# Performance work log

Hardware: AMD Instinct MI355X
Metric: run time of the kernel (lower is better)

Reference implementation:

```python
import jax, jax.numpy as jnp
import numpy as np

B, S, D, H = 4, 2048, 1024, 16
DH = D // H  # 64


def setup_inputs() -> dict:
    key = jax.random.key(0)
    ks = jax.random.split(key, 9)
    scale = 1.0 / np.sqrt(D)
    x = jax.random.normal(ks[0], (B, S, D), dtype=jnp.float32)
    # Stacked per-head projection weights, equivalent to ModuleList of Linear(D, DH)
    Wq = jax.random.uniform(ks[1], (H, D, DH), jnp.float32, -scale, scale)
    bq = jax.random.uniform(ks[2], (H, DH), jnp.float32, -scale, scale)
    Wk = jax.random.uniform(ks[3], (H, D, DH), jnp.float32, -scale, scale)
    bk = jax.random.uniform(ks[4], (H, DH), jnp.float32, -scale, scale)
    Wv = jax.random.uniform(ks[5], (H, D, DH), jnp.float32, -scale, scale)
    bv = jax.random.uniform(ks[6], (H, DH), jnp.float32, -scale, scale)
    Wo = jax.random.uniform(ks[7], (D, D), jnp.float32, -scale, scale)
    bo = jax.random.uniform(ks[8], (D,), jnp.float32, -scale, scale)
    return {"x": x, "Wq": Wq, "bq": bq, "Wk": Wk, "bk": bk,
            "Wv": Wv, "bv": bv, "Wo": Wo, "bo": bo}


def reference(x, Wq, bq, Wk, bk, Wv, bv, Wo, bo):
    # Per-head Linear projections, batched across heads: [B,S,D]x[H,D,DH] -> [B,H,S,DH]
    q = jnp.einsum('bsd,hde->bhse', x, Wq) + bq[None, :, None, :]
    k = jnp.einsum('bsd,hde->bhse', x, Wk) + bk[None, :, None, :]
    v = jnp.einsum('bsd,hde->bhse', x, Wv) + bv[None, :, None, :]
    # Scaled dot-product attention (no mask is applied in the original forward)
    scores = jnp.einsum('bhse,bhte->bhst', q, k) / jnp.sqrt(jnp.float32(DH))
    attn = jax.nn.softmax(scores, axis=-1)
    z = jnp.einsum('bhst,bhte->bhse', attn, v)  # [B,H,S,DH]
    # Concat heads on last dim (head-major order matches torch.cat over dim=-1)
    multihead = jnp.transpose(z, (0, 2, 1, 3)).reshape(B, S, D)
    return multihead @ Wo + bo
```

## Files before the change

kernel.cpp:

```cpp
#include <hip/hip_runtime.h>
#include <hip/hip_bf16.h>
#include <cstdint>
#include <cstddef>


typedef unsigned short u16;
typedef unsigned int u32;
typedef __attribute__((ext_vector_type(8))) __bf16 bf16x8;
typedef __attribute__((ext_vector_type(8))) unsigned short u16x8;
typedef __attribute__((ext_vector_type(4))) float f32x4;
typedef __attribute__((ext_vector_type(4))) unsigned int u32x4;

__device__ __forceinline__ u16 f2bf(float f) {
  union { __hip_bfloat16 h; u16 u; } c;
  c.h = __float2bfloat16(f);
  return c.u;
}
__device__ __forceinline__ u32 pk2c(float a, float b) {
  const u32 ua = __float_as_uint(a);
  const u32 ub = __float_as_uint(b);
  const u32 ra = ua + 0x7FFFu + ((ua >> 16) & 1u);
  const u32 rb = ub + 0x7FFFu + ((ub >> 16) & 1u);
  return (ra >> 16) | (rb & 0xFFFF0000u);
}
__device__ __forceinline__ float ex2(float x) {
  return __builtin_amdgcn_exp2f(x);
}

__device__ __forceinline__ void async16(const void* g, void* l) {
  __builtin_amdgcn_global_load_lds(
      (const __attribute__((address_space(1))) void*)g,
      (__attribute__((address_space(3))) void*)l, 16, 0, 0);
}

__global__ void k_pack_all(const float* __restrict__ x,
                           const float* __restrict__ Wq, const float* __restrict__ Wk,
                           const float* __restrict__ Wv,
                           const float* __restrict__ bq, const float* __restrict__ bk,
                           const float* __restrict__ bv,
                           const float* __restrict__ Wo,
                           u16* __restrict__ xb, u16* __restrict__ Wt,
                           float* __restrict__ bqkv, u16* __restrict__ Wot) {
  const int bid = blockIdx.x;
  if (bid < 8192) {
    const int i = (bid * 256 + threadIdx.x) * 4;
    const float4 v = *(const float4*)(x + i);
    ushort4 o;
    o.x = f2bf(v.x); o.y = f2bf(v.y); o.z = f2bf(v.z); o.w = f2bf(v.w);
    *(ushort4*)(xb + i) = o;
  } else if (bid < 11264) {
    const int gid = (bid - 8192) * 256 + threadIdx.x;
    const int n = gid >> 8;
    const int d0 = (gid & 255) << 2;
    const int proj = n >> 10, rem = n & 1023, h = rem >> 6, e = rem & 63;
    const float* Wp = (proj == 0) ? Wq : ((proj == 1) ? Wk : Wv);
    const float* src = Wp + h * 65536 + e;
    ushort4 o;
    o.x = f2bf(src[(d0 + 0) * 64]);
    o.y = f2bf(src[(d0 + 1) * 64]);
    o.z = f2bf(src[(d0 + 2) * 64]);
    o.w = f2bf(src[(d0 + 3) * 64]);
    *(ushort4*)(Wt + (size_t)n * 1024 + d0) = o;
  } else if (bid < 11276) {
    const int n = (bid - 11264) * 256 + threadIdx.x;
    const int proj = n >> 10, rem = n & 1023, h = rem >> 6, e = rem & 63;
    const float* bp = (proj == 0) ? bq : ((proj == 1) ? bk : bv);
    bqkv[n] = bp[h * 64 + e];
  } else {
    const int gid = (bid - 11276) * 256 + threadIdx.x;
    const int n = gid >> 8;
    const int d0 = (gid & 255) << 2;
    ushort4 o;
    o.x = f2bf(Wo[(size_t)(d0 + 0) * 1024 + n]);
    o.y = f2bf(Wo[(size_t)(d0 + 1) * 1024 + n]);
    o.z = f2bf(Wo[(size_t)(d0 + 2) * 1024 + n]);
    o.w = f2bf(Wo[(size_t)(d0 + 3) * 1024 + n]);
    *(ushort4*)(Wot + (size_t)n * 1024 + d0) = o;
  }
}

template <int MODE>
__global__ __launch_bounds__(256)
void k_gemm(const u16* __restrict__ A, const u16* __restrict__ Bt,
            const float* __restrict__ bias, void* __restrict__ Cout, int ldc) {
  __shared__ __align__(16) u16 Alds[128 * 32];
  __shared__ __align__(16) u16 Blds[128 * 32];
  const int t = threadIdx.x;
  const int lane = t & 63;
  const int w = t >> 6;
  const int l15 = lane & 15;
  const int quad = lane >> 4;
  const int wm = w >> 1, wn = w & 1;
  const int m0 = blockIdx.y << 7;
  const int n0 = blockIdx.x << 7;

  const u16* ga0 = A + (size_t)(m0 + (t >> 2)) * 1024 + (t & 3) * 8;
  const u16* ga1 = ga0 + (size_t)64 * 1024;
  const u16* gb0 = Bt + (size_t)(n0 + (t >> 2)) * 1024 + (t & 3) * 8;
  const u16* gb1 = gb0 + (size_t)64 * 1024;
  u16* const lA0 = Alds + w * 512;
  u16* const lA1 = Alds + w * 512 + 2048;
  u16* const lB0 = Blds + w * 512;
  u16* const lB1 = Blds + w * 512 + 2048;

  f32x4 acc[4][4];
#pragma unroll
  for (int mi = 0; mi < 4; ++mi)
#pragma unroll
    for (int ni = 0; ni < 4; ++ni) acc[mi][ni] = (f32x4){0.f, 0.f, 0.f, 0.f};

  for (int k0 = 0; k0 < 1024; k0 += 32) {
    __syncthreads();
    async16(ga0, lA0); async16(ga1, lA1);
    async16(gb0, lB0); async16(gb1, lB1);
    ga0 += 32; ga1 += 32; gb0 += 32; gb1 += 32;
    __syncthreads();
    bf16x8 af[4], bfr[4];
#pragma unroll
    for (int i = 0; i < 4; ++i) {
      af[i]  = *(const bf16x8*)(Alds + (wm * 64 + i * 16 + l15) * 32 + quad * 8);
      bfr[i] = *(const bf16x8*)(Blds + (wn * 64 + i * 16 + l15) * 32 + quad * 8);
    }
#pragma unroll
    for (int mi = 0; mi < 4; ++mi)
#pragma unroll
      for (int ni = 0; ni < 4; ++ni)
        acc[mi][ni] = __builtin_amdgcn_mfma_f32_16x16x32_bf16(af[mi], bfr[ni], acc[mi][ni], 0, 0, 0);
  }

  const int row0 = m0 + wm * 64;
  const int col0 = n0 + wn * 64;
  const float qscale = (MODE == 0 && col0 < 1024) ? 0.125f * 1.4426950408889634f : 1.0f;
#pragma unroll
  for (int mi = 0; mi < 4; ++mi) {
#pragma unroll
    for (int ni = 0; ni < 4; ++ni) {
      const int col = col0 + ni * 16 + l15;
      const float bb = bias[col];
#pragma unroll
      for (int r = 0; r < 4; ++r) {
        const int row = row0 + mi * 16 + quad * 4 + r;
        const float v = (acc[mi][ni][r] + bb) * qscale;
        if (MODE == 0) ((u16*)Cout)[(size_t)row * ldc + col] = f2bf(v);
        else           ((float*)Cout)[(size_t)row * ldc + col] = v;
      }
    }
  }
}

__global__ __launch_bounds__(256)
void k_vt(const u16* __restrict__ qkv, u16* __restrict__ vtg) {
  __shared__ u16 tile[64][72];
  const int t = threadIdx.x;
  const int bh = blockIdx.y, b = bh >> 4, h = bh & 15;
  const int s0 = blockIdx.x << 6;
  {
    const int row = t >> 2, col0 = (t & 3) * 16;
    const u16* src = qkv + (size_t)(b * 2048 + s0 + row) * 3072 + 2048 + h * 64 + col0;
    const u16x8 v0 = *(const u16x8*)src;
    const u16x8 v1 = *(const u16x8*)(src + 8);
    *(u16x8*)&tile[row][col0] = v0;
    *(u16x8*)&tile[row][col0 + 8] = v1;
  }
  __syncthreads();
  {
    const int e = t >> 2, sc = (t & 3) * 16;
    u16 buf[16];
#pragma unroll
    for (int i = 0; i < 16; ++i) buf[i] = tile[sc + i][e];
    u16* dst = vtg + ((size_t)bh * 64 + e) * 2048 + s0 + sc;
    *(u16x8*)dst = *(const u16x8*)&buf[0];
    *(u16x8*)(dst + 8) = *(const u16x8*)&buf[8];
  }
}

__global__ __launch_bounds__(256)
void k_attn(const u16* __restrict__ qkv, const u16* __restrict__ vtg,
            u16* __restrict__ mh) {
  __shared__ __align__(16) u16 smem[16384];
  u16* const Klds = smem;
  u16* const Vlds = smem + 8192;

  const int t = threadIdx.x;
  const int lane = t & 63;
  const int w = t >> 6;
  const int l15 = lane & 15;
  const int quad = lane >> 4;
  const int bh = blockIdx.y, b = bh >> 4, h = bh & 15;
  const int s0 = blockIdx.x << 7;

  const int lam0 = t >> 3;
  const int key0 = (lam0 & 3) | (((lam0 >> 2) & 3) << 3) | (((lam0 >> 4) & 1) << 2);
  const int ck = (t & 7) ^ (lam0 & 7);
  const u16* kbase = qkv + (size_t)(b * 2048 + key0) * 3072 + 1024 + h * 64 + ck * 8;
  const int e0 = t >> 4;
  const int cv = (t & 15) ^ e0;
  const u16* vbase = vtg + ((size_t)bh * 64 + e0) * 2048 + cv * 8;
  u16* const KldsW = Klds + w * 512;
  u16* const VldsW = Vlds + w * 512;

  bf16x8 aq[2][2];
#pragma unroll
  for (int g = 0; g < 2; ++g)
#pragma unroll
    for (int ks2 = 0; ks2 < 2; ++ks2)
      aq[g][ks2] = *(const bf16x8*)(qkv +
          (size_t)(b * 2048 + s0 + w * 32 + g * 16 + l15) * 3072 +
          h * 64 + ks2 * 32 + quad * 8);

  const u32x4 onesu = (u32x4){0x3F803F80u, 0x3F803F80u, 0x3F803F80u, 0x3F803F80u};
  const bf16x8 ones = __builtin_bit_cast(bf16x8, onesu);

  f32x4 o[2][4];
  f32x4 lacc[2];
#pragma unroll
  for (int g = 0; g < 2; ++g) {
    lacc[g] = (f32x4){0.f, 0.f, 0.f, 0.f};
#pragma unroll
    for (int ne = 0; ne < 4; ++ne) o[g][ne] = (f32x4){0.f, 0.f, 0.f, 0.f};
  }

  for (int kt = 0; kt < 16; ++kt) {
    __syncthreads();
#pragma unroll
    for (int r = 0; r < 4; ++r)
      async16(kbase + r * (32 * 3072), KldsW + r * 2048);
#pragma unroll
    for (int r = 0; r < 4; ++r)
      async16(vbase + r * (16 * 2048), VldsW + r * 2048);
    kbase += 128 * 3072;
    vbase += 128;
    __syncthreads();

#pragma unroll
    for (int ks = 0; ks < 4; ++ks) {
      u32x4 pf[2];
#pragma unroll
      for (int h2 = 0; h2 < 2; ++h2) {
        const int kt8 = ks * 2 + h2;
        const int row = kt8 * 16 + l15;
        const bf16x8 kf0 = *(const bf16x8*)(Klds + row * 64 + ((quad) ^ (l15 & 7)) * 8);
        const bf16x8 kf1 = *(const bf16x8*)(Klds + row * 64 + ((4 + quad) ^ (l15 & 7)) * 8);
        f32x4 st[2];
#pragma unroll
        for (int g = 0; g < 2; ++g) {
          st[g] = __builtin_amdgcn_mfma_f32_16x16x32_bf16(kf0, aq[g][0], (f32x4){0.f,0.f,0.f,0.f}, 0, 0, 0);
          st[g] = __builtin_amdgcn_mfma_f32_16x16x32_bf16(kf1, aq[g][1], st[g], 0, 0, 0);
        }
#pragma unroll
        for (int g = 0; g < 2; ++g) {
          const float p0 = ex2(st[g][0]), p1 = ex2(st[g][1]);
          const float p2 = ex2(st[g][2]), p3 = ex2(st[g][3]);
          pf[g][h2 * 2 + 0] = pk2c(p0, p1);
          pf[g][h2 * 2 + 1] = pk2c(p2, p3);
        }
      }
#pragma unroll
      for (int ne = 0; ne < 4; ++ne) {
        const int e = ne * 16 + l15;
        const bf16x8 bv8 = *(const bf16x8*)(Vlds + e * 128 + (((ks * 4 + quad) ^ l15) & 15) * 8);
#pragma unroll
        for (int g = 0; g < 2; ++g)
          o[g][ne] = __builtin_amdgcn_mfma_f32_16x16x32_bf16(
              __builtin_bit_cast(bf16x8, pf[g]), bv8, o[g][ne], 0, 0, 0);
      }
#pragma unroll
      for (int g = 0; g < 2; ++g)
        lacc[g] = __builtin_amdgcn_mfma_f32_16x16x32_bf16(
            __builtin_bit_cast(bf16x8, pf[g]), ones, lacc[g], 0, 0, 0);
    }
  }

#pragma unroll
  for (int g = 0; g < 2; ++g) {
#pragma unroll
    for (int r = 0; r < 4; ++r) {
      const float iv = 1.f / lacc[g][r];
      const int row = s0 + w * 32 + g * 16 + quad * 4 + r;
#pragma unroll
      for (int ne = 0; ne < 4; ++ne) {
        const int col = h * 64 + ne * 16 + l15;
        mh[(size_t)(b * 2048 + row) * 1024 + col] = f2bf(o[g][ne][r] * iv);
      }
    }
  }
}

extern "C" void kernel_launch(void* const* d_in, const int* in_sizes, int n_in,
                              void* d_out, int out_size, void* d_ws, size_t ws_size,
                              hipStream_t stream) {
  (void)in_sizes; (void)n_in; (void)out_size; (void)ws_size;
  const float* x  = (const float*)d_in[0];
  const float* Wq = (const float*)d_in[1];
  const float* bq = (const float*)d_in[2];
  const float* Wk = (const float*)d_in[3];
  const float* bk = (const float*)d_in[4];
  const float* Wv = (const float*)d_in[5];
  const float* bv = (const float*)d_in[6];
  const float* Wo = (const float*)d_in[7];
  const float* bo = (const float*)d_in[8];

  char* ws = (char*)d_ws;
  u16*   Xb   = (u16*)  (ws + 0);
  u16*   Vtg  = (u16*)  (ws + 0);
  u16*   Wt   = (u16*)  (ws + 16777216);
  float* bqkv = (float*)(ws + 23068672);
  u16*   Wot  = (u16*)  (ws + 23080960);
  u16*   QKV  = (u16*)  (ws + 25178112);
  u16*   MH   = (u16*)  (ws + 75509760);
  float* out  = (float*)d_out;

  k_pack_all <<<12300, 256, 0, stream>>>(x, Wq, Wk, Wv, bq, bk, bv, Wo,
                                         Xb, Wt, bqkv, Wot);
  k_gemm<0>  <<<dim3(24, 64), 256, 0, stream>>>(Xb, Wt, bqkv, (void*)QKV, 3072);
  k_vt       <<<dim3(32, 64), 256, 0, stream>>>(QKV, Vtg);
  k_attn     <<<dim3(16, 64), 256, 0, stream>>>(QKV, Vtg, MH);
  k_gemm<1>  <<<dim3(8, 64), 256, 0, stream>>>(MH, Wot, bo, (void*)out, 1024);
}
```

Before: 319.5 us.

## Transpose weights via LDS tiles, use packed bf16 convert, reorder attention grid

The weight pack step now transposes Wq/Wk/Wv and Wo through a 64x64 shared-memory tile, so global reads and writes are coalesced instead of strided scalar loads. The bf16 pair-pack helper uses the hardware packed-convert builtin when the compiler provides it. The attention grid is swapped so that consecutive blocks cover different (batch, head) pairs for the same query tile, which changes how work is spread across CUs and what the caches see. Rounding behavior of the builtin may differ slightly from the manual rounding on special values.

After: 291.7 us. 8.7% less time.

```diff
diff --git a/kernel.cpp b/kernel.cpp
--- a/kernel.cpp
+++ b/kernel.cpp
@@ -16,12 +16,21 @@
   c.h = __float2bfloat16(f);
   return c.u;
 }
+#if defined(__has_builtin)
+#if __has_builtin(__builtin_amdgcn_cvt_pk_bf16_f32)
+#define HAS_PK_BF16 1
+#endif
+#endif
 __device__ __forceinline__ u32 pk2c(float a, float b) {
+#ifdef HAS_PK_BF16
+  return __builtin_bit_cast(u32, __builtin_amdgcn_cvt_pk_bf16_f32(a, b));
+#else
   const u32 ua = __float_as_uint(a);
   const u32 ub = __float_as_uint(b);
   const u32 ra = ua + 0x7FFFu + ((ua >> 16) & 1u);
   const u32 rb = ub + 0x7FFFu + ((ub >> 16) & 1u);
   return (ra >> 16) | (rb & 0xFFFF0000u);
+#endif
 }
 __device__ __forceinline__ float ex2(float x) {
   return __builtin_amdgcn_exp2f(x);
@@ -41,41 +50,61 @@
                            const float* __restrict__ Wo,
                            u16* __restrict__ xb, u16* __restrict__ Wt,
                            float* __restrict__ bqkv, u16* __restrict__ Wot) {
+  __shared__ __align__(16) u16 tile[64][72];
   const int bid = blockIdx.x;
-  if (bid < 8192) {
-    const int i = (bid * 256 + threadIdx.x) * 4;
+  const int t = threadIdx.x;
+  if (bid < 1024) {
+    const float* src;
+    u16* dstp;
+    int rstride, n_base, d0;
+    if (bid < 768) {
+      const int proj = bid >> 8, h = (bid >> 4) & 15, dt = bid & 15;
+      const float* Wp = (proj == 0) ? Wq : ((proj == 1) ? Wk : Wv);
+      src = Wp + h * 65536 + (dt * 64) * 64;
+      rstride = 64;
+      n_base = proj * 1024 + h * 64;
+      d0 = dt * 64;
+      dstp = Wt;
+    } else {
+      const int tb = bid - 768, nt = tb >> 4, dt = tb & 15;
+      src = Wo + (size_t)(dt * 64) * 1024 + nt * 64;
+      rstride = 1024;
+      n_base = nt * 64;
+      d0 = dt * 64;
+      dstp = Wot;
+    }
+    {
+      const int row = t >> 2, c0 = (t & 3) * 16;
+      const float* s = src + row * rstride + c0;
+#pragma unroll
+      for (int j = 0; j < 4; ++j) {
+        const float4 v = *(const float4*)(s + j * 4);
+        ushort4 o;
+        o.x = f2bf(v.x); o.y = f2bf(v.y); o.z = f2bf(v.z); o.w = f2bf(v.w);
+        *(ushort4*)&tile[row][c0 + j * 4] = o;
+      }
+    }
+    __syncthreads();
+    {
+      const int e = t >> 2, c0 = (t & 3) * 16;
+      u16 buf[16];
+#pragma unroll
+      for (int i = 0; i < 16; ++i) buf[i] = tile[c0 + i][e];
+      u16* d = dstp + (size_t)(n_base + e) * 1024 + d0 + c0;
+      *(u16x8*)d = *(const u16x8*)&buf[0];
+      *(u16x8*)(d + 8) = *(const u16x8*)&buf[8];
+    }
+  } else if (bid < 9216) {
+    const int i = ((bid - 1024) * 256 + t) * 4;
     const float4 v = *(const float4*)(x + i);
     ushort4 o;
     o.x = f2bf(v.x); o.y = f2bf(v.y); o.z = f2bf(v.z); o.w = f2bf(v.w);
     *(ushort4*)(xb + i) = o;
-  } else if (bid < 11264) {
-    const int gid = (bid - 8192) * 256 + threadIdx.x;
-    const int n = gid >> 8;
-    const int d0 = (gid & 255) << 2;
-    const int proj = n >> 10, rem = n & 1023, h = rem >> 6, e = rem & 63;
-    const float* Wp = (proj == 0) ? Wq : ((proj == 1) ? Wk : Wv);
-    const float* src = Wp + h * 65536 + e;
-    ushort4 o;
-    o.x = f2bf(src[(d0 + 0) * 64]);
-    o.y = f2bf(src[(d0 + 1) * 64]);
-    o.z = f2bf(src[(d0 + 2) * 64]);
-    o.w = f2bf(src[(d0 + 3) * 64]);
-    *(ushort4*)(Wt + (size_t)n * 1024 + d0) = o;
-  } else if (bid < 11276) {
-    const int n = (bid - 11264) * 256 + threadIdx.x;
+  } else {
+    const int n = (bid - 9216) * 256 + t;
     const int proj = n >> 10, rem = n & 1023, h = rem >> 6, e = rem & 63;
     const float* bp = (proj == 0) ? bq : ((proj == 1) ? bk : bv);
     bqkv[n] = bp[h * 64 + e];
-  } else {
-    const int gid = (bid - 11276) * 256 + threadIdx.x;
-    const int n = gid >> 8;
-    const int d0 = (gid & 255) << 2;
-    ushort4 o;
-    o.x = f2bf(Wo[(size_t)(d0 + 0) * 1024 + n]);
-    o.y = f2bf(Wo[(size_t)(d0 + 1) * 1024 + n]);
-    o.z = f2bf(Wo[(size_t)(d0 + 2) * 1024 + n]);
-    o.w = f2bf(Wo[(size_t)(d0 + 3) * 1024 + n]);
-    *(ushort4*)(Wot + (size_t)n * 1024 + d0) = o;
   }
 }
 
@@ -186,8 +215,8 @@
   const int w = t >> 6;
   const int l15 = lane & 15;
   const int quad = lane >> 4;
-  const int bh = blockIdx.y, b = bh >> 4, h = bh & 15;
-  const int s0 = blockIdx.x << 7;
+  const int bh = blockIdx.x, b = bh >> 4, h = bh & 15;
+  const int s0 = blockIdx.y << 7;
 
   const int lam0 = t >> 3;
   const int key0 = (lam0 & 3) | (((lam0 >> 2) & 3) << 3) | (((lam0 >> 4) & 1) << 2);
@@ -310,10 +339,10 @@
   u16*   MH   = (u16*)  (ws + 75509760);
   float* out  = (float*)d_out;
 
-  k_pack_all <<<12300, 256, 0, stream>>>(x, Wq, Wk, Wv, bq, bk, bv, Wo,
-                                         Xb, Wt, bqkv, Wot);
+  k_pack_all <<<9228, 256, 0, stream>>>(x, Wq, Wk, Wv, bq, bk, bv, Wo,
+                                        Xb, Wt, bqkv, Wot);
   k_gemm<0>  <<<dim3(24, 64), 256, 0, stream>>>(Xb, Wt, bqkv, (void*)QKV, 3072);
   k_vt       <<<dim3(32, 64), 256, 0, stream>>>(QKV, Vtg);
-  k_attn     <<<dim3(16, 64), 256, 0, stream>>>(QKV, Vtg, MH);
+  k_attn     <<<dim3(64, 16), 256, 0, stream>>>(QKV, Vtg, MH);
   k_gemm<1>  <<<dim3(8, 64), 256, 0, stream>>>(MH, Wot, bo, (void*)out, 1024);
 }
```
